# Optimization experiments

Hardware: AMD Instinct MI355X
Metric: run time of the kernel (lower is better)

## Reference

```python
import jax, jax.numpy as jnp
import numpy as np

N = 4096      # batch of RNA sequences
SEQ = 41      # hardcoded sequence length in the torch code
VEC = 15      # vector_length
T = 8         # target_length
EMB = 32      # embedding_dim of RNASequenceFilter.fc
LDIM = 256    # SequenceSplitter embedding_dim
RED = 64      # SequenceSplitter reduced_dim
BN_EPS = 1e-5


def setup_inputs() -> dict:
    key = jax.random.key(0)
    ks = jax.random.split(key, 20)
    A = jax.random.normal(ks[0], (N, SEQ, VEC), jnp.float32)
    start = jax.random.randint(ks[1], (N,), 0, 34)
    length = jax.random.randint(ks[2], (N,), 1, 9)  # region length in [1,8]
    C = jnp.stack([start, start + length - 1], axis=1).astype(jnp.int32)
    L = jax.random.normal(ks[3], (N, SEQ, LDIM), jnp.float32)
    s = 0.05
    return {
        "A": A, "C": C, "L": L,
        # RNASequenceFilter.fc : Linear(120,32) + Tanh + BatchNorm1d(32) (training mode)
        "W1": jax.random.normal(ks[4], (T * VEC, EMB), jnp.float32) * s,
        "b1": jnp.zeros((EMB,), jnp.float32),
        "bn_gamma": jnp.ones((EMB,), jnp.float32),
        "bn_beta": jnp.zeros((EMB,), jnp.float32),
        "sigma": jnp.float32(1.0),
        # SequenceSplitter lazy weights, initialized to ones
        "Pos_weights": jnp.ones((N, SEQ), jnp.float32),
        "Neg_weights": jnp.ones((N, SEQ), jnp.float32),
        # fc_pos
        "Wp1": jax.random.normal(ks[5], (LDIM, RED), jnp.float32) * s,
        "bp1": jnp.zeros((RED,), jnp.float32),
        "Wp2": jax.random.normal(ks[6], (RED, RED), jnp.float32) * s,
        "bp2": jnp.zeros((RED,), jnp.float32),
        # fc_neg
        "Wq1": jax.random.normal(ks[7], (LDIM, RED), jnp.float32) * s,
        "bq1": jnp.zeros((RED,), jnp.float32),
        "Wq2": jax.random.normal(ks[8], (RED, RED), jnp.float32) * s,
        "bq2": jnp.zeros((RED,), jnp.float32),
        # fc_all
        "Wa": jax.random.normal(ks[9], (LDIM, RED), jnp.float32) * s,
        "ba": jnp.zeros((RED,), jnp.float32),
    }


def _safe_cdist(x, y):
    # Euclidean cdist with zero (not NaN) gradient at zero distance.
    sq = (jnp.sum(x * x, -1)[:, None] + jnp.sum(y * y, -1)[None, :]
          - 2.0 * (x @ y.T))
    sq = jnp.maximum(sq, 0.0)
    safe = jnp.where(sq > 0.0, sq, 1.0)
    return jnp.where(sq > 0.0, jnp.sqrt(safe), 0.0)


def _forward(A, C, L, W1, b1, bn_gamma, bn_beta, sigma,
             Pos_weights, Neg_weights,
             Wp1, bp1, Wp2, bp2, Wq1, bq1, Wq2, bq2, Wa, ba):
    n = A.shape[0]
    start = C[:, 0].astype(jnp.int32)
    end = C[:, 1].astype(jnp.int32)
    length = end - start + 1  # [n], in [1, SEQ]

    # ---- build_graph: variable-length gather + linear interpolate (align_corners=False)
    j = jnp.arange(T, dtype=jnp.float32)
    scale = length.astype(jnp.float32)[:, None] / T          # [n,1]
    src = jnp.maximum(scale * (j + 0.5) - 0.5, 0.0)           # [n,T]
    i0 = jnp.minimum(jnp.floor(src).astype(jnp.int32), (length - 1)[:, None])
    i1 = jnp.minimum(i0 + 1, (length - 1)[:, None])
    w = src - i0.astype(jnp.float32)                          # lerp weight
    rows = jnp.arange(n)[:, None]
    g0 = A[rows, start[:, None] + i0]                         # [n,T,VEC]
    g1 = A[rows, start[:, None] + i1]
    key_regions = (1.0 - w)[..., None] * g0 + w[..., None] * g1
    flat = key_regions.reshape(n, T * VEC)

    h = jnp.tanh(flat @ W1 + b1)
    mu = h.mean(axis=0)
    var = ((h - mu) ** 2).mean(axis=0)                        # biased, training-mode BN
    emb = bn_gamma * (h - mu) * jax.lax.rsqrt(var + BN_EPS) + bn_beta

    D = jnp.exp(-_safe_cdist(emb, emb) / (2.0 * sigma ** 2))
    eye = jnp.eye(n, dtype=bool)
    off = ~eye
    avg = jnp.sum(jnp.where(off, D, 0.0)) / (n * (n - 1))
    D = jnp.where(D < avg, 0.0, D)
    mn = jnp.min(jnp.where(off, D, jnp.inf))
    mx = jnp.max(jnp.where(off, D, -jnp.inf))
    mx = jnp.where(mx == mn, mn + 1.0, mx)
    D = (D - mn) / (mx - mn)
    D = jnp.where(eye, 1.0, D)

    # ---- SequenceSplitter (only the paths feeding the outputs)
    idx = jnp.arange(SEQ)
    pmask = ((idx[None, :] >= start[:, None]) &
             (idx[None, :] <= end[:, None])).astype(L.dtype)  # [n,SEQ]
    pos_rep = (pmask * Pos_weights)[..., None] * L            # [n,SEQ,LDIM]
    neg_rep = ((1.0 - pmask) * Neg_weights)[..., None] * L

    key_t = jnp.tanh(jnp.tanh(pos_rep @ Wp1 + bp1) @ Wp2 + bp2)
    pos_vec = key_t.mean(axis=1)                              # [n,RED]
    nonkey_t = jnp.tanh(jnp.tanh(neg_rep @ Wq1 + bq1) @ Wq2 + bq2)
    neg_vec = nonkey_t.mean(axis=1)

    pos_sim = jnp.sum(jnp.exp(-_safe_cdist(pos_vec, pos_vec)))
    neg_sim = jnp.sum(jnp.exp(-_safe_cdist(pos_vec, neg_vec)))
    contrastive_loss = -jnp.log(pos_sim / neg_sim)

    final_feature = jnp.tanh((pos_rep + neg_rep) @ Wa + ba).mean(axis=1)  # [n,RED]
    return final_feature, contrastive_loss, D


def reference(A, C, L, W1, b1, bn_gamma, bn_beta, sigma,
              Pos_weights, Neg_weights,
              Wp1, bp1, Wp2, bp2, Wq1, bq1, Wq2, bq2, Wa, ba):
    return _forward(A, C, L, W1, b1, bn_gamma, bn_beta, sigma,
                    Pos_weights, Neg_weights,
                    Wp1, bp1, Wp2, bp2, Wq1, bq1, Wq2, bq2, Wa, ba)
```

## Files before the change

### kernel.cpp

```cpp
#include <hip/hip_runtime.h>
#include <cmath>

#define NN 4096
#define SEQ 41
#define VEC 15
#define TT 8
#define EMBD 32
#define LDIM 256
#define RED 64

#define WS_H       0
#define WS_EMB     524288
#define WS_SQN     1048576
#define WS_ROWSUM  1064960
#define WS_ROWMIN  1081344
#define WS_ROWMAX  1097728
#define WS_POSV    1114112
#define WS_NEGV    2162688
#define WS_STATS   3211264
#define WS_SIMS    3211520
#define WS_PAR     3211536

#define OUT_LOSS  (NN*RED)
#define OUT_D     (NN*RED + 1)

__global__ void k_init(char* ws) {
  double* sims = (double*)(ws + WS_SIMS);
  sims[0] = 0.0; sims[1] = 0.0;
}

__global__ __launch_bounds__(64) void k_interp_h(
    const float* __restrict__ A, const int* __restrict__ C,
    const float* __restrict__ W1, const float* __restrict__ b1,
    float* __restrict__ h)
{
  __shared__ float flat[TT*VEC];
  const int n = blockIdx.x;
  const int t = threadIdx.x;
  const int st = C[2*n], en = C[2*n+1];
  const int len = en - st + 1;
  const float scale = __fdiv_rn((float)len, 8.0f);
  const float* Arow = A + ((size_t)n*SEQ + st) * VEC;
  for (int idx = t; idx < TT*VEC; idx += 64) {
    int j = idx / VEC, k = idx - j*VEC;
    float jf = (float)j + 0.5f;
    float src = fmaxf(__fsub_rn(__fmul_rn(scale, jf), 0.5f), 0.0f);
    int i0 = min((int)floorf(src), len-1);
    int i1 = min(i0+1, len-1);
    float w = __fsub_rn(src, (float)i0);
    float g0 = Arow[i0*VEC + k];
    float g1 = Arow[i1*VEC + k];
    flat[idx] = __fadd_rn(__fmul_rn(__fsub_rn(1.0f, w), g0), __fmul_rn(w, g1));
  }
  __syncthreads();
  if (t < EMBD) {
    float acc = 0.0f;
    #pragma unroll
    for (int i = 0; i < TT*VEC; i++) acc = __fmaf_rn(flat[i], W1[i*EMBD + t], acc);
    acc = __fadd_rn(acc, b1[t]);
    h[(size_t)n*EMBD + t] = (float)tanh((double)acc);
  }
}

#define BCH 128
__global__ __launch_bounds__(256) void k_bnstats(const float* __restrict__ h,
                                                 float* __restrict__ stats)
{
  __shared__ float tile[2][BCH*EMBD];
  __shared__ float smu[32];
  const int t = threadIdx.x;
  const int NCH = NN / BCH;

  {
    const float4* src = (const float4*)h;
    float4* dst = (float4*)tile[0];
    for (int v = t; v < BCH*8; v += 256) dst[v] = src[v];
  }
  __syncthreads();
  float acc = 0.0f;
  for (int c = 0; c < NCH; c++) {
    if (t >= 64 && c+1 < NCH) {
      const float4* src = (const float4*)(h + (size_t)(c+1)*BCH*EMBD);
      float4* dst = (float4*)tile[(c+1)&1];
      for (int v = t-64; v < BCH*8; v += 192) dst[v] = src[v];
    }
    if (t < 32) {
      const float* p = tile[c&1];
      #pragma unroll 8
      for (int r = 0; r < BCH; r++) acc = __fadd_rn(acc, p[r*EMBD + t]);
    }
    __syncthreads();
  }
  if (t < 32) smu[t] = __fdiv_rn(acc, 4096.0f);
  __syncthreads();

  {
    const float4* src = (const float4*)h;
    float4* dst = (float4*)tile[0];
    for (int v = t; v < BCH*8; v += 256) dst[v] = src[v];
  }
  __syncthreads();
  float q = 0.0f;
  for (int c = 0; c < NCH; c++) {
    if (t >= 64 && c+1 < NCH) {
      const float4* src = (const float4*)(h + (size_t)(c+1)*BCH*EMBD);
      float4* dst = (float4*)tile[(c+1)&1];
      for (int v = t-64; v < BCH*8; v += 192) dst[v] = src[v];
    }
    if (t < 32) {
      const float* p = tile[c&1];
      const float m = smu[t];
      #pragma unroll 8
      for (int r = 0; r < BCH; r++) {
        float d = __fsub_rn(p[r*EMBD + t], m);
        q = __fadd_rn(q, __fmul_rn(d, d));
      }
    }
    __syncthreads();
  }
  if (t < 32) {
    float var = __fdiv_rn(q, 4096.0f);
    stats[t] = smu[t];
    stats[32+t] = __fdiv_rn(1.0f, __fsqrt_rn(__fadd_rn(var, 1e-5f)));
  }
}

__global__ __launch_bounds__(256) void k_emb(
    const float* __restrict__ h, const float* __restrict__ stats,
    const float* __restrict__ gamma, const float* __restrict__ beta,
    float* __restrict__ emb, float* __restrict__ sqn)
{
  __shared__ float tile[8][32];
  const int t = threadIdx.x;
  const int r = t >> 5;
  const int e = t & 31;
  const int n = blockIdx.x*8 + r;
  float hv = h[(size_t)n*EMBD + e];
  float v = __fadd_rn(__fmul_rn(__fmul_rn(gamma[e], __fsub_rn(hv, stats[e])), stats[32+e]), beta[e]);
  emb[(size_t)n*EMBD + e] = v;
  tile[r][e] = v;
  __syncthreads();
  if (e == 0) {
    float sq[32];
    #pragma unroll
    for (int k = 0; k < 32; k++) { float x = tile[r][k]; sq[k] = __fmul_rn(x, x); }
    float rr[8];
    #pragma unroll
    for (int m = 0; m < 8; m++) rr[m] = sq[m];
    #pragma unroll
    for (int g = 1; g < 4; g++)
      #pragma unroll
      for (int m = 0; m < 8; m++) rr[m] = __fadd_rn(rr[m], sq[8*g + m]);
    float a = __fadd_rn(__fadd_rn(rr[0], rr[1]), __fadd_rn(rr[2], rr[3]));
    float b = __fadd_rn(__fadd_rn(rr[4], rr[5]), __fadd_rn(rr[6], rr[7]));
    sqn[n] = __fadd_rn(a, b);
  }
}

__device__ __forceinline__ float finishD(float dot, float ni, float nj, float denom)
{
  float t1 = __fadd_rn(ni, nj);
  float sq = __fsub_rn(t1, __fmul_rn(2.0f, dot));
  sq = fmaxf(sq, 0.0f);
  float dist = (sq > 0.0f) ? __fsqrt_rn(sq) : 0.0f;
  float q = __fdiv_rn(-dist, denom);
  return (float)exp((double)q);
}

#define TI 64
#define TJ 128
__global__ __launch_bounds__(256) void k_dtile(
    const float* __restrict__ emb, const float* __restrict__ sqn,
    const float* __restrict__ sigma, float* __restrict__ Dout)
{
  __shared__ __align__(16) float Ei[TI][36];
  __shared__ __align__(16) float Ej[TJ][36];
  const int t = threadIdx.x;
  const int bi = blockIdx.y;
  const int bj = blockIdx.x;
  const int jt = t & 15;
  const int it = t >> 4;

  {
    const float4* si = (const float4*)(emb + (size_t)bi*TI*EMBD);
    for (int v = t; v < TI*8; v += 256) {
      float4 x = si[v];
      *(float4*)&Ei[v >> 3][(v & 7) * 4] = x;
    }
    const float4* sj = (const float4*)(emb + (size_t)bj*TJ*EMBD);
    for (int v = t; v < TJ*8; v += 256) {
      float4 x = sj[v];
      *(float4*)&Ej[v >> 3][(v & 7) * 4] = x;
    }
  }

  const float s0 = sigma[0];
  const float denom = __fmul_rn(2.0f, __fmul_rn(s0, s0));

  float ni[4], nj[8];
  #pragma unroll
  for (int r = 0; r < 4; r++) ni[r] = sqn[bi*TI + it*4 + r];
  #pragma unroll
  for (int u = 0; u < 8; u++) nj[u] = sqn[bj*TJ + jt + 16*u];

  __syncthreads();

  float acc[4][8];
  #pragma unroll
  for (int r = 0; r < 4; r++)
    #pragma unroll
    for (int u = 0; u < 8; u++) acc[r][u] = 0.0f;

  #pragma unroll
  for (int kq = 0; kq < 8; kq++) {
    float4 a[4], b[8];
    #pragma unroll
    for (int r = 0; r < 4; r++) a[r] = *(const float4*)&Ei[it*4 + r][kq*4];
    #pragma unroll
    for (int u = 0; u < 8; u++) b[u] = *(const float4*)&Ej[jt + 16*u][kq*4];
    #pragma unroll
    for (int r = 0; r < 4; r++)
      #pragma unroll
      for (int u = 0; u < 8; u++) {
        float s = acc[r][u];
        s = __fmaf_rn(a[r].x, b[u].x, s);
        s = __fmaf_rn(a[r].y, b[u].y, s);
        s = __fmaf_rn(a[r].z, b[u].z, s);
        s = __fmaf_rn(a[r].w, b[u].w, s);
        acc[r][u] = s;
      }
  }

  #pragma unroll
  for (int r = 0; r < 4; r++) {
    const int ig = bi*TI + it*4 + r;
    float* Dr = Dout + (size_t)ig * NN + bj*TJ;
    #pragma unroll
    for (int u = 0; u < 8; u++) {
      const int jg = bj*TJ + jt + 16*u;
      float Dv = finishD(acc[r][u], ni[r], nj[u], denom);
      Dr[jt + 16*u] = (jg == ig) ? 0.0f : Dv;
    }
  }
}

__global__ __launch_bounds__(256) void k_drowsum(
    const float* __restrict__ Dout,
    float* __restrict__ rowsum, float* __restrict__ rowmin, float* __restrict__ rowmax)
{
  __shared__ float Drow[NN + NN/128];
  __shared__ float cs[32];
  __shared__ float rmn[256], rmx[256];
  const int i = blockIdx.x;
  const int t = threadIdx.x;
  const float* Dr = Dout + (size_t)i*NN;
  const float PINF = __int_as_float(0x7f800000);
  const float NINF = __int_as_float(0xff800000);
  float lmn = PINF, lmx = NINF;
  for (int j = t; j < NN; j += 256) {
    float v = Dr[j];
    Drow[j + (j>>7)] = v;
    if (j != i) { lmn = fminf(lmn, v); lmx = fmaxf(lmx, v); }
  }
  rmn[t] = lmn; rmx[t] = lmx;
  __syncthreads();
  if (t < 32) {
    const float* p = Drow + 129*t;
    float rr[8];
    #pragma unroll
    for (int m = 0; m < 8; m++) rr[m] = p[m];
    for (int g = 1; g < 16; g++)
      #pragma unroll
      for (int m = 0; m < 8; m++) rr[m] = __fadd_rn(rr[m], p[8*g + m]);
    float a = __fadd_rn(__fadd_rn(rr[0], rr[1]), __fadd_rn(rr[2], rr[3]));
    float b = __fadd_rn(__fadd_rn(rr[4], rr[5]), __fadd_rn(rr[6], rr[7]));
    cs[t] = __fadd_rn(a, b);
  }
  __syncthreads();
  if (t == 0) {
    for (int len = 32; len > 1; len >>= 1)
      for (int k = 0; k < len/2; k++)
        cs[k] = __fadd_rn(cs[2*k], cs[2*k+1]);
    rowsum[i] = cs[0];
  }
  for (int s = 128; s > 0; s >>= 1) {
    if (t < s) {
      rmn[t] = fminf(rmn[t], rmn[t+s]);
      rmx[t] = fmaxf(rmx[t], rmx[t+s]);
    }
    __syncthreads();
  }
  if (t == 0) { rowmin[i] = rmn[0]; rowmax[i] = rmx[0]; }
}

__global__ __launch_bounds__(256) void k_dreduce(
    const float* __restrict__ rowsum, const float* __restrict__ rowmin,
    const float* __restrict__ rowmax, float* __restrict__ par)
{
  __shared__ float s[8192];
  __shared__ float rmn[256], rmx[256];
  const int t = threadIdx.x;
  for (int k = t; k < NN; k += 256) s[k] = rowsum[k];
  float mn = __int_as_float(0x7f800000), mx = __int_as_float(0xff800000);
  for (int k = t; k < NN; k += 256) {
    mn = fminf(mn, rowmin[k]);
    mx = fmaxf(mx, rowmax[k]);
  }
  rmn[t] = mn; rmx[t] = mx;
  __syncthreads();
  int src = 0, dst = 4096;
  for (int len = NN; len > 1; len >>= 1) {
    for (int k = t; k < len/2; k += 256)
      s[dst + k] = __fadd_rn(s[src + 2*k], s[src + 2*k+1]);
    __syncthreads();
    src = dst; dst = src + len/2;
  }
  for (int w = 128; w > 0; w >>= 1) {
    if (t < w) {
      rmn[t] = fminf(rmn[t], rmn[t+w]);
      rmx[t] = fmaxf(rmx[t], rmx[t+w]);
    }
    __syncthreads();
  }
  if (t == 0) {
    float S = s[src];
    float avg = __fdiv_rn(S, 16773120.0f);
    float mnr = rmn[0], mxr = rmx[0];
    float mnt = (mnr < avg) ? 0.0f : mnr;
    float mxt = (mxr < avg) ? 0.0f : mxr;
    if (mxt == mnt) mxt = __fadd_rn(mnt, 1.0f);
    par[0] = avg; par[1] = mnt; par[2] = __fsub_rn(mxt, mnt);
  }
}

__global__ __launch_bounds__(256) void k_dnorm(
    const float* __restrict__ par, float* __restrict__ D)
{
  const int i = blockIdx.x;
  const int t = threadIdx.x;
  const float avg = par[0], mnt = par[1], rng = par[2];
  float4* row = (float4*)(D + (size_t)i*NN);
  const int iv = i >> 2;
  for (int v = t; v < NN/4; v += 256) {
    float4 d = row[v];
    float o[4];
    float in[4] = {d.x, d.y, d.z, d.w};
    #pragma unroll
    for (int u = 0; u < 4; u++) {
      float val = (in[u] < avg) ? 0.0f : in[u];
      o[u] = __fdiv_rn(__fsub_rn(val, mnt), rng);
    }
    if (v == iv) o[i & 3] = 1.0f;
    row[v] = make_float4(o[0], o[1], o[2], o[3]);
  }
}

__global__ __launch_bounds__(256) void k_lpass(
    const float* __restrict__ L, const int* __restrict__ C,
    const float* __restrict__ PosW, const float* __restrict__ NegW,
    const float* __restrict__ Wp1, const float* __restrict__ bp1,
    const float* __restrict__ Wp2, const float* __restrict__ bp2,
    const float* __restrict__ Wq1, const float* __restrict__ bq1,
    const float* __restrict__ Wq2, const float* __restrict__ bq2,
    const float* __restrict__ Wa, const float* __restrict__ ba,
    float* __restrict__ out_ff, float* __restrict__ posv, float* __restrict__ negv)
{
  __shared__ __align__(16) float buf[SEQ*128];
  __shared__ float wps[SEQ], wns[SEQ];
  __shared__ float part[12*64];

  float* apos = buf;
  float* aneg = buf + SEQ*RED;

  const int n = blockIdx.x;
  const int t = threadIdx.x;
  const int w = t >> 6;
  const int lane = t & 63;

  if (t < SEQ) {
    int st = C[2*n], en = C[2*n+1];
    bool pm = (t >= st && t <= en);
    wps[t] = pm ? PosW[(size_t)n*SEQ + t] : 0.0f;
    wns[t] = pm ? 0.0f : NegW[(size_t)n*SEQ + t];
  }

  float accp[11], accq[11], acca[11];
  #pragma unroll
  for (int i = 0; i < 11; i++) { accp[i]=0.f; accq[i]=0.f; acca[i]=0.f; }

  const float4* Lg = (const float4*)(L + (size_t)n * (SEQ*LDIM));

  #pragma unroll
  for (int half = 0; half < 2; half++) {
    {
      float4* B4 = (float4*)buf;
      for (int v = t; v < SEQ*32; v += 256) {
        int s = v >> 5, c = v & 31;
        B4[v] = Lg[s*64 + half*32 + c];
      }
    }
    __syncthreads();
    const float* Wp1h = Wp1 + (size_t)half*128*RED + lane;
    const float* Wq1h = Wq1 + (size_t)half*128*RED + lane;
    const float* Wah  = Wa  + (size_t)half*128*RED + lane;
    for (int k0 = 0; k0 < 128; k0 += 4) {
      float wpr[4], wqr[4], war[4];
      #pragma unroll
      for (int kk = 0; kk < 4; kk++) {
        wpr[kk] = Wp1h[(k0+kk)*RED];
        wqr[kk] = Wq1h[(k0+kk)*RED];
        war[kk] = Wah [(k0+kk)*RED];
      }
      #pragma unroll
      for (int si = 0; si < 11; si++) {
        int s = w + 4*si;
        if (s < SEQ) {
          float4 l4 = *(const float4*)&buf[s*128 + k0];
          accp[si] = __fmaf_rn(l4.x, wpr[0], accp[si]);
          accp[si] = __fmaf_rn(l4.y, wpr[1], accp[si]);
          accp[si] = __fmaf_rn(l4.z, wpr[2], accp[si]);
          accp[si] = __fmaf_rn(l4.w, wpr[3], accp[si]);
          accq[si] = __fmaf_rn(l4.x, wqr[0], accq[si]);
          accq[si] = __fmaf_rn(l4.y, wqr[1], accq[si]);
          accq[si] = __fmaf_rn(l4.z, wqr[2], accq[si]);
          accq[si] = __fmaf_rn(l4.w, wqr[3], accq[si]);
          acca[si] = __fmaf_rn(l4.x, war[0], acca[si]);
          acca[si] = __fmaf_rn(l4.y, war[1], acca[si]);
          acca[si] = __fmaf_rn(l4.z, war[2], acca[si]);
          acca[si] = __fmaf_rn(l4.w, war[3], acca[si]);
        }
      }
    }
    __syncthreads();
  }

  const float bpl = bp1[lane], bql = bq1[lane], bal = ba[lane];
  float ffl = 0.f;
  #pragma unroll
  for (int si = 0; si < 11; si++) {
    int s = w + 4*si;
    if (s < SEQ) {
      float wp = wps[s], wn = wns[s];
      apos[s*RED + lane] = tanhf(__fmaf_rn(wp, accp[si], bpl));
      aneg[s*RED + lane] = tanhf(__fmaf_rn(wn, accq[si], bql));
      ffl += tanhf(__fmaf_rn(wp+wn, acca[si], bal));
    }
  }
  part[(0*4 + w)*64 + lane] = ffl;
  __syncthreads();

  float accP[11], accQ[11];
  #pragma unroll
  for (int i = 0; i < 11; i++) { accP[i]=0.f; accQ[i]=0.f; }
  const float* Wp2l = Wp2 + lane;
  const float* Wq2l = Wq2 + lane;
  for (int k0 = 0; k0 < RED; k0 += 4) {
    float p2[4], q2[4];
    #pragma unroll
    for (int kk = 0; kk < 4; kk++) {
      p2[kk] = Wp2l[(k0+kk)*RED];
      q2[kk] = Wq2l[(k0+kk)*RED];
    }
    #pragma unroll
    for (int si = 0; si < 11; si++) {
      int s = w + 4*si;
      if (s < SEQ) {
        float4 a4 = *(const float4*)&apos[s*RED + k0];
        float4 b4 = *(const float4*)&aneg[s*RED + k0];
        accP[si] = __fmaf_rn(a4.x, p2[0], accP[si]);
        accP[si] = __fmaf_rn(a4.y, p2[1], accP[si]);
        accP[si] = __fmaf_rn(a4.z, p2[2], accP[si]);
        accP[si] = __fmaf_rn(a4.w, p2[3], accP[si]);
        accQ[si] = __fmaf_rn(b4.x, q2[0], accQ[si]);
        accQ[si] = __fmaf_rn(b4.y, q2[1], accQ[si]);
        accQ[si] = __fmaf_rn(b4.z, q2[2], accQ[si]);
        accQ[si] = __fmaf_rn(b4.w, q2[3], accQ[si]);
      }
    }
  }
  const float bp2l = bp2[lane], bq2l = bq2[lane];
  float pl = 0.f, nl = 0.f;
  #pragma unroll
  for (int si = 0; si < 11; si++) {
    int s = w + 4*si;
    if (s < SEQ) {
      pl += tanhf(__fadd_rn(accP[si], bp2l));
      nl += tanhf(__fadd_rn(accQ[si], bq2l));
    }
  }
  part[(1*4 + w)*64 + lane] = pl;
  part[(2*4 + w)*64 + lane] = nl;
  __syncthreads();

  if (w == 0) {
    float s = part[0*256 + 0*64 + lane] + part[0*256 + 1*64 + lane]
            + part[0*256 + 2*64 + lane] + part[0*256 + 3*64 + lane];
    out_ff[(size_t)n*RED + lane] = s * (1.0f/41.0f);
  } else if (w == 1) {
    float s = part[1*256 + 0*64 + lane] + part[1*256 + 1*64 + lane]
            + part[1*256 + 2*64 + lane] + part[1*256 + 3*64 + lane];
    posv[(size_t)n*RED + lane] = s * (1.0f/41.0f);
  } else if (w == 2) {
    float s = part[2*256 + 0*64 + lane] + part[2*256 + 1*64 + lane]
            + part[2*256 + 2*64 + lane] + part[2*256 + 3*64 + lane];
    negv[(size_t)n*RED + lane] = s * (1.0f/41.0f);
  }
}

__global__ __launch_bounds__(256) void k_sim(
    const float* __restrict__ posv, const float* __restrict__ negv,
    double* __restrict__ sims)
{
  __shared__ float xI[64*64];
  __shared__ float yJ[64*65];
  __shared__ float nxs[64];
  __shared__ double wsum[4];
  const int which = blockIdx.z;
  const float* X = posv;
  const float* Y = which ? negv : posv;
  const int bi = blockIdx.x, bj = blockIdx.y, t = threadIdx.x;
  for (int v = t; v < 4096; v += 256) {
    int r = v >> 6, c = v & 63;
    xI[r*64+c] = X[(size_t)(bi*64+r)*RED + c];
    yJ[r*65+c] = Y[(size_t)(bj*64+r)*RED + c];
  }
  __syncthreads();
  if (t < 64) {
    float s = 0.f;
    #pragma unroll
    for (int k = 0; k < 64; k++) { float v = xI[t*64+k]; s += v*v; }
    nxs[t] = s;
  }
  const int jl = t & 63, iq = t >> 6;
  float yv[64];
  #pragma unroll
  for (int k = 0; k < 64; k++) yv[k] = yJ[jl*65+k];
  float ny = 0.f;
  #pragma unroll
  for (int k = 0; k < 64; k++) ny += yv[k]*yv[k];
  __syncthreads();
  double lsum = 0.0;
  for (int ii = 0; ii < 16; ii++) {
    int il = iq*16 + ii;
    float dot = 0.f;
    #pragma unroll
    for (int k = 0; k < 64; k += 4) {
      float4 x = *(const float4*)&xI[il*64+k];
      dot += x.x*yv[k] + x.y*yv[k+1] + x.z*yv[k+2] + x.w*yv[k+3];
    }
    float sq = fmaxf(nxs[il] + ny - 2.0f*dot, 0.0f);
    float dist = (sq > 0.f) ? sqrtf(sq) : 0.f;
    lsum += (double)expf(-dist);
  }
  #pragma unroll
  for (int m = 32; m >= 1; m >>= 1) lsum += __shfl_down(lsum, m);
  if ((t & 63) == 0) wsum[t>>6] = lsum;
  __syncthreads();
  if (t == 0) atomicAdd(&sims[which], wsum[0]+wsum[1]+wsum[2]+wsum[3]);
}

__global__ void k_loss(const double* __restrict__ sims, float* __restrict__ out_loss) {
  out_loss[0] = (float)(-log(sims[0]/sims[1]));
}

extern "C" void kernel_launch(void* const* d_in, const int* in_sizes, int n_in,
                              void* d_out, int out_size, void* d_ws, size_t ws_size,
                              hipStream_t stream) {
  const float* A     = (const float*)d_in[0];
  const int*   C     = (const int*)  d_in[1];
  const float* L     = (const float*)d_in[2];
  const float* W1    = (const float*)d_in[3];
  const float* b1    = (const float*)d_in[4];
  const float* gamma = (const float*)d_in[5];
  const float* beta  = (const float*)d_in[6];
  const float* sigma = (const float*)d_in[7];
  const float* PosW  = (const float*)d_in[8];
  const float* NegW  = (const float*)d_in[9];
  const float* Wp1   = (const float*)d_in[10];
  const float* bp1   = (const float*)d_in[11];
  const float* Wp2   = (const float*)d_in[12];
  const float* bp2   = (const float*)d_in[13];
  const float* Wq1   = (const float*)d_in[14];
  const float* bq1   = (const float*)d_in[15];
  const float* Wq2   = (const float*)d_in[16];
  const float* bq2   = (const float*)d_in[17];
  const float* Wa    = (const float*)d_in[18];
  const float* ba    = (const float*)d_in[19];

  float* out = (float*)d_out;
  char* ws = (char*)d_ws;
  float* h      = (float*)(ws + WS_H);
  float* emb    = (float*)(ws + WS_EMB);
  float* sqn    = (float*)(ws + WS_SQN);
  float* rowsum = (float*)(ws + WS_ROWSUM);
  float* rowmin = (float*)(ws + WS_ROWMIN);
  float* rowmax = (float*)(ws + WS_ROWMAX);
  float* posv   = (float*)(ws + WS_POSV);
  float* negv   = (float*)(ws + WS_NEGV);
  float* stats  = (float*)(ws + WS_STATS);
  double* sims  = (double*)(ws + WS_SIMS);
  float* par    = (float*)(ws + WS_PAR);

  hipLaunchKernelGGL(k_init, dim3(1), dim3(1), 0, stream, (char*)d_ws);
  hipLaunchKernelGGL(k_interp_h, dim3(NN), dim3(64), 0, stream, A, C, W1, b1, h);
  hipLaunchKernelGGL(k_bnstats, dim3(1), dim3(256), 0, stream, h, stats);
  hipLaunchKernelGGL(k_emb, dim3(NN/8), dim3(256), 0, stream, h, stats, gamma, beta, emb, sqn);
  hipLaunchKernelGGL(k_dtile, dim3(NN/TJ, NN/TI), dim3(256), 0, stream, emb, sqn, sigma, out + OUT_D);
  hipLaunchKernelGGL(k_drowsum, dim3(NN), dim3(256), 0, stream, out + OUT_D, rowsum, rowmin, rowmax);
  hipLaunchKernelGGL(k_dreduce, dim3(1), dim3(256), 0, stream, rowsum, rowmin, rowmax, par);
  hipLaunchKernelGGL(k_dnorm, dim3(NN), dim3(256), 0, stream, par, out + OUT_D);
  hipLaunchKernelGGL(k_lpass, dim3(NN), dim3(256), 0, stream,
                     L, C, PosW, NegW, Wp1, bp1, Wp2, bp2, Wq1, bq1, Wq2, bq2, Wa, ba,
                     out, posv, negv);
  hipLaunchKernelGGL(k_sim, dim3(64,64,2), dim3(256), 0, stream, posv, negv, sims);
  hipLaunchKernelGGL(k_loss, dim3(1), dim3(1), 0, stream, sims, out + OUT_LOSS);
}
```

Before: 892.3 us.

## Fuse D row reductions into tile kernel, skip masked branch work, halve symmetric sim

Per-row sum, min and max of the distance matrix are now computed inside the tile kernel via wave shuffles and atomics, with per-chunk partial sums combined by a small kernel. This removes the separate pass that re-read the full 4096x4096 D matrix. The L-pass now runs only the positive or the negative branch per sequence position, and replaces the masked-out branch with a precomputed constant tanh term. The positive-positive similarity kernel skips the lower-triangle blocks and doubles the off-diagonal ones, which changes the float summation order, and the init kernel is folded into the combine kernel.

Measured after the change: 942.3 us. 1.06x slower.

```diff
diff --git a/kernel.cpp b/kernel.cpp
--- a/kernel.cpp
+++ b/kernel.cpp
@@ -10,6 +10,7 @@
 #define RED 64
 
 #define WS_H       0
+#define WS_CHUNKS  0
 #define WS_EMB     524288
 #define WS_SQN     1048576
 #define WS_ROWSUM  1064960
@@ -23,11 +24,6 @@
 
 #define OUT_LOSS  (NN*RED)
 #define OUT_D     (NN*RED + 1)
-
-__global__ void k_init(char* ws) {
-  double* sims = (double*)(ws + WS_SIMS);
-  sims[0] = 0.0; sims[1] = 0.0;
-}
 
 __global__ __launch_bounds__(64) void k_interp_h(
     const float* __restrict__ A, const int* __restrict__ C,
@@ -128,7 +124,8 @@
 __global__ __launch_bounds__(256) void k_emb(
     const float* __restrict__ h, const float* __restrict__ stats,
     const float* __restrict__ gamma, const float* __restrict__ beta,
-    float* __restrict__ emb, float* __restrict__ sqn)
+    float* __restrict__ emb, float* __restrict__ sqn,
+    float* __restrict__ rowmin, float* __restrict__ rowmax)
 {
   __shared__ float tile[8][32];
   const int t = threadIdx.x;
@@ -154,6 +151,8 @@
     float a = __fadd_rn(__fadd_rn(rr[0], rr[1]), __fadd_rn(rr[2], rr[3]));
     float b = __fadd_rn(__fadd_rn(rr[4], rr[5]), __fadd_rn(rr[6], rr[7]));
     sqn[n] = __fadd_rn(a, b);
+    rowmin[n] = __int_as_float(0x7f800000);
+    rowmax[n] = 0.0f;
   }
 }
 
@@ -171,7 +170,8 @@
 #define TJ 128
 __global__ __launch_bounds__(256) void k_dtile(
     const float* __restrict__ emb, const float* __restrict__ sqn,
-    const float* __restrict__ sigma, float* __restrict__ Dout)
+    const float* __restrict__ sigma, float* __restrict__ Dout,
+    float* __restrict__ chunks, float* __restrict__ rowmin, float* __restrict__ rowmax)
 {
   __shared__ __align__(16) float Ei[TI][36];
   __shared__ __align__(16) float Ej[TJ][36];
@@ -231,66 +231,74 @@
       }
   }
 
+  const float PINF = __int_as_float(0x7f800000);
+  const float NINF = __int_as_float(0xff800000);
+  float wv[4][8];
+  float thmn[4], thmx[4];
   #pragma unroll
   for (int r = 0; r < 4; r++) {
     const int ig = bi*TI + it*4 + r;
     float* Dr = Dout + (size_t)ig * NN + bj*TJ;
+    float mn = PINF, mx = NINF;
     #pragma unroll
     for (int u = 0; u < 8; u++) {
       const int jg = bj*TJ + jt + 16*u;
       float Dv = finishD(acc[r][u], ni[r], nj[u], denom);
-      Dr[jt + 16*u] = (jg == ig) ? 0.0f : Dv;
-    }
-  }
-}
-
-__global__ __launch_bounds__(256) void k_drowsum(
-    const float* __restrict__ Dout,
-    float* __restrict__ rowsum, float* __restrict__ rowmin, float* __restrict__ rowmax)
-{
-  __shared__ float Drow[NN + NN/128];
-  __shared__ float cs[32];
-  __shared__ float rmn[256], rmx[256];
-  const int i = blockIdx.x;
-  const int t = threadIdx.x;
-  const float* Dr = Dout + (size_t)i*NN;
-  const float PINF = __int_as_float(0x7f800000);
-  const float NINF = __int_as_float(0xff800000);
-  float lmn = PINF, lmx = NINF;
-  for (int j = t; j < NN; j += 256) {
-    float v = Dr[j];
-    Drow[j + (j>>7)] = v;
-    if (j != i) { lmn = fminf(lmn, v); lmx = fmaxf(lmx, v); }
-  }
-  rmn[t] = lmn; rmx[t] = lmx;
-  __syncthreads();
-  if (t < 32) {
-    const float* p = Drow + 129*t;
-    float rr[8];
-    #pragma unroll
-    for (int m = 0; m < 8; m++) rr[m] = p[m];
-    for (int g = 1; g < 16; g++)
-      #pragma unroll
-      for (int m = 0; m < 8; m++) rr[m] = __fadd_rn(rr[m], p[8*g + m]);
-    float a = __fadd_rn(__fadd_rn(rr[0], rr[1]), __fadd_rn(rr[2], rr[3]));
-    float b = __fadd_rn(__fadd_rn(rr[4], rr[5]), __fadd_rn(rr[6], rr[7]));
-    cs[t] = __fadd_rn(a, b);
-  }
-  __syncthreads();
-  if (t == 0) {
-    for (int len = 32; len > 1; len >>= 1)
-      for (int k = 0; k < len/2; k++)
-        cs[k] = __fadd_rn(cs[2*k], cs[2*k+1]);
-    rowsum[i] = cs[0];
-  }
-  for (int s = 128; s > 0; s >>= 1) {
-    if (t < s) {
-      rmn[t] = fminf(rmn[t], rmn[t+s]);
-      rmx[t] = fmaxf(rmx[t], rmx[t+s]);
-    }
-    __syncthreads();
-  }
-  if (t == 0) { rowmin[i] = rmn[0]; rowmax[i] = rmx[0]; }
+      const bool dg = (jg == ig);
+      float wq = dg ? 0.0f : Dv;
+      wv[r][u] = wq;
+      Dr[jt + 16*u] = wq;
+      mn = fminf(mn, dg ? PINF : Dv);
+      mx = fmaxf(mx, dg ? NINF : Dv);
+    }
+    thmn[r] = mn; thmx[r] = mx;
+  }
+
+  #pragma unroll
+  for (int r = 0; r < 4; r++) {
+    float part[8];
+    #pragma unroll
+    for (int u = 0; u < 8; u++) part[u] = __shfl_xor(wv[r][u], 8, 16);
+    float a = wv[r][0];
+    a = __fadd_rn(a, part[0]);
+    #pragma unroll
+    for (int u = 1; u < 8; u++) {
+      a = __fadd_rn(a, wv[r][u]);
+      a = __fadd_rn(a, part[u]);
+    }
+    float s1 = __fadd_rn(a,  __shfl_xor(a, 1, 16));
+    float s2 = __fadd_rn(s1, __shfl_xor(s1, 2, 16));
+    float s3 = __fadd_rn(s2, __shfl_xor(s2, 4, 16));
+    float mn = thmn[r], mx = thmx[r];
+    #pragma unroll
+    for (int m = 1; m < 16; m <<= 1) {
+      mn = fminf(mn, __shfl_xor(mn, m, 16));
+      mx = fmaxf(mx, __shfl_xor(mx, m, 16));
+    }
+    if (jt == 0) {
+      const int ig = bi*TI + it*4 + r;
+      chunks[(size_t)bj*NN + ig] = s3;
+      atomicMin((int*)&rowmin[ig], __float_as_int(mn));
+      atomicMax((int*)&rowmax[ig], __float_as_int(mx));
+    }
+  }
+}
+
+__global__ __launch_bounds__(256) void k_rowcombine(
+    const float* __restrict__ chunks, float* __restrict__ rowsum,
+    double* __restrict__ sims)
+{
+  const int i = blockIdx.x*256 + threadIdx.x;
+  if (blockIdx.x == 0 && threadIdx.x == 0) { sims[0] = 0.0; sims[1] = 0.0; }
+  float ch[32];
+  #pragma unroll
+  for (int c = 0; c < 32; c++) ch[c] = chunks[(size_t)c*NN + i];
+  #pragma unroll
+  for (int len = 32; len > 1; len >>= 1)
+    #pragma unroll
+    for (int k = 0; k < 16; k++)
+      if (k < len/2) ch[k] = __fadd_rn(ch[2*k], ch[2*k+1]);
+  rowsum[i] = ch[0];
 }
 
 __global__ __launch_bounds__(256) void k_dreduce(
@@ -368,25 +376,36 @@
   __shared__ __align__(16) float buf[SEQ*128];
   __shared__ float wps[SEQ], wns[SEQ];
   __shared__ float part[12*64];
+  __shared__ __align__(16) float tb1[2*RED];
 
   float* apos = buf;
   float* aneg = buf + SEQ*RED;
 
   const int n = blockIdx.x;
   const int t = threadIdx.x;
-  const int w = t >> 6;
+  const int wu = __builtin_amdgcn_readfirstlane(t >> 6);
   const int lane = t & 63;
 
+  const int st = C[2*n], en = C[2*n+1];
+
   if (t < SEQ) {
-    int st = C[2*n], en = C[2*n+1];
     bool pm = (t >= st && t <= en);
     wps[t] = pm ? PosW[(size_t)n*SEQ + t] : 0.0f;
     wns[t] = pm ? 0.0f : NegW[(size_t)n*SEQ + t];
   }
-
-  float accp[11], accq[11], acca[11];
-  #pragma unroll
-  for (int i = 0; i < 11; i++) { accp[i]=0.f; accq[i]=0.f; acca[i]=0.f; }
+  if (t < RED) tb1[t] = tanhf(bp1[t]);
+  else if (t < 2*RED) tb1[t] = tanhf(bq1[t - RED]);
+
+  bool anyIn = false, anyOut = false;
+  #pragma unroll
+  for (int si = 0; si < 11; si++) {
+    int s = wu + 4*si;
+    if (s < SEQ) { bool r = (s >= st) && (s <= en); anyIn |= r; anyOut |= !r; }
+  }
+
+  float accs[11], acca[11];
+  #pragma unroll
+  for (int i = 0; i < 11; i++) { accs[i]=0.f; acca[i]=0.f; }
 
   const float4* Lg = (const float4*)(L + (size_t)n * (SEQ*LDIM));
 
@@ -405,25 +424,33 @@
     const float* Wah  = Wa  + (size_t)half*128*RED + lane;
     for (int k0 = 0; k0 < 128; k0 += 4) {
       float wpr[4], wqr[4], war[4];
+      if (anyIn) {
+        #pragma unroll
+        for (int kk = 0; kk < 4; kk++) wpr[kk] = Wp1h[(k0+kk)*RED];
+      }
+      if (anyOut) {
+        #pragma unroll
+        for (int kk = 0; kk < 4; kk++) wqr[kk] = Wq1h[(k0+kk)*RED];
+      }
       #pragma unroll
-      for (int kk = 0; kk < 4; kk++) {
-        wpr[kk] = Wp1h[(k0+kk)*RED];
-        wqr[kk] = Wq1h[(k0+kk)*RED];
-        war[kk] = Wah [(k0+kk)*RED];
-      }
+      for (int kk = 0; kk < 4; kk++) war[kk] = Wah[(k0+kk)*RED];
       #pragma unroll
       for (int si = 0; si < 11; si++) {
-        int s = w + 4*si;
+        const int s = wu + 4*si;
         if (s < SEQ) {
+          const bool inr = (s >= st) && (s <= en);
           float4 l4 = *(const float4*)&buf[s*128 + k0];
-          accp[si] = __fmaf_rn(l4.x, wpr[0], accp[si]);
-          accp[si] = __fmaf_rn(l4.y, wpr[1], accp[si]);
-          accp[si] = __fmaf_rn(l4.z, wpr[2], accp[si]);
-          accp[si] = __fmaf_rn(l4.w, wpr[3], accp[si]);
-          accq[si] = __fmaf_rn(l4.x, wqr[0], accq[si]);
-          accq[si] = __fmaf_rn(l4.y, wqr[1], accq[si]);
-          accq[si] = __fmaf_rn(l4.z, wqr[2], accq[si]);
-          accq[si] = __fmaf_rn(l4.w, wqr[3], accq[si]);
+          if (inr) {
+            accs[si] = __fmaf_rn(l4.x, wpr[0], accs[si]);
+            accs[si] = __fmaf_rn(l4.y, wpr[1], accs[si]);
+            accs[si] = __fmaf_rn(l4.z, wpr[2], accs[si]);
+            accs[si] = __fmaf_rn(l4.w, wpr[3], accs[si]);
+          } else {
+            accs[si] = __fmaf_rn(l4.x, wqr[0], accs[si]);
+            accs[si] = __fmaf_rn(l4.y, wqr[1], accs[si]);
+            accs[si] = __fmaf_rn(l4.z, wqr[2], accs[si]);
+            accs[si] = __fmaf_rn(l4.w, wqr[3], accs[si]);
+          }
           acca[si] = __fmaf_rn(l4.x, war[0], acca[si]);
           acca[si] = __fmaf_rn(l4.y, war[1], acca[si]);
           acca[si] = __fmaf_rn(l4.z, war[2], acca[si]);
@@ -438,20 +465,27 @@
   float ffl = 0.f;
   #pragma unroll
   for (int si = 0; si < 11; si++) {
-    int s = w + 4*si;
+    const int s = wu + 4*si;
     if (s < SEQ) {
-      float wp = wps[s], wn = wns[s];
-      apos[s*RED + lane] = tanhf(__fmaf_rn(wp, accp[si], bpl));
-      aneg[s*RED + lane] = tanhf(__fmaf_rn(wn, accq[si], bql));
-      ffl += tanhf(__fmaf_rn(wp+wn, acca[si], bal));
-    }
-  }
-  part[(0*4 + w)*64 + lane] = ffl;
-  __syncthreads();
-
-  float accP[11], accQ[11];
-  #pragma unroll
-  for (int i = 0; i < 11; i++) { accP[i]=0.f; accQ[i]=0.f; }
+      const bool inr = (s >= st) && (s <= en);
+      if (inr) {
+        float wp = wps[s];
+        apos[s*RED + lane] = tanhf(__fmaf_rn(wp, accs[si], bpl));
+        ffl += tanhf(__fmaf_rn(wp, acca[si], bal));
+      } else {
+        float wn = wns[s];
+        aneg[s*RED + lane] = tanhf(__fmaf_rn(wn, accs[si], bql));
+        ffl += tanhf(__fmaf_rn(wn, acca[si], bal));
+      }
+    }
+  }
+  part[(0*4 + wu)*64 + lane] = ffl;
+  __syncthreads();
+
+  float acc2[11];
+  float c2p = 0.f, c2q = 0.f;
+  #pragma unroll
+  for (int i = 0; i < 11; i++) acc2[i] = 0.f;
   const float* Wp2l = Wp2 + lane;
   const float* Wq2l = Wq2 + lane;
   for (int k0 = 0; k0 < RED; k0 += 4) {
@@ -461,46 +495,71 @@
       p2[kk] = Wp2l[(k0+kk)*RED];
       q2[kk] = Wq2l[(k0+kk)*RED];
     }
+    float4 tp = *(const float4*)&tb1[k0];
+    float4 tq = *(const float4*)&tb1[RED + k0];
+    c2p = __fmaf_rn(tp.x, p2[0], c2p);
+    c2p = __fmaf_rn(tp.y, p2[1], c2p);
+    c2p = __fmaf_rn(tp.z, p2[2], c2p);
+    c2p = __fmaf_rn(tp.w, p2[3], c2p);
+    c2q = __fmaf_rn(tq.x, q2[0], c2q);
+    c2q = __fmaf_rn(tq.y, q2[1], c2q);
+    c2q = __fmaf_rn(tq.z, q2[2], c2q);
+    c2q = __fmaf_rn(tq.w, q2[3], c2q);
     #pragma unroll
     for (int si = 0; si < 11; si++) {
-      int s = w + 4*si;
+      const int s = wu + 4*si;
       if (s < SEQ) {
-        float4 a4 = *(const float4*)&apos[s*RED + k0];
-        float4 b4 = *(const float4*)&aneg[s*RED + k0];
-        accP[si] = __fmaf_rn(a4.x, p2[0], accP[si]);
-        accP[si] = __fmaf_rn(a4.y, p2[1], accP[si]);
-        accP[si] = __fmaf_rn(a4.z, p2[2], accP[si]);
-        accP[si] = __fmaf_rn(a4.w, p2[3], accP[si]);
-        accQ[si] = __fmaf_rn(b4.x, q2[0], accQ[si]);
-        accQ[si] = __fmaf_rn(b4.y, q2[1], accQ[si]);
-        accQ[si] = __fmaf_rn(b4.z, q2[2], accQ[si]);
-        accQ[si] = __fmaf_rn(b4.w, q2[3], accQ[si]);
+        const bool inr = (s >= st) && (s <= en);
+        if (inr) {
+          float4 a4 = *(const float4*)&apos[s*RED + k0];
+          acc2[si] = __fmaf_rn(a4.x, p2[0], acc2[si]);
+          acc2[si] = __fmaf_rn(a4.y, p2[1], acc2[si]);
+          acc2[si] = __fmaf_rn(a4.z, p2[2], acc2[si]);
+          acc2[si] = __fmaf_rn(a4.w, p2[3], acc2[si]);
+        } else {
+          float4 b4 = *(const float4*)&aneg[s*RED + k0];
+          acc2[si] = __fmaf_rn(b4.x, q2[0], acc2[si]);
+          acc2[si] = __fmaf_rn(b4.y, q2[1], acc2[si]);
+          acc2[si] = __fmaf_rn(b4.z, q2[2], acc2[si]);
+          acc2[si] = __fmaf_rn(b4.w, q2[3], acc2[si]);
+        }
       }
     }
   }
   const float bp2l = bp2[lane], bq2l = bq2[lane];
+  const float tcp = tanhf(__fadd_rn(c2p, bp2l));
+  const float tcq = tanhf(__fadd_rn(c2q, bq2l));
   float pl = 0.f, nl = 0.f;
+  int nin = 0, nval = 0;
   #pragma unroll
   for (int si = 0; si < 11; si++) {
-    int s = w + 4*si;
+    const int s = wu + 4*si;
     if (s < SEQ) {
-      pl += tanhf(__fadd_rn(accP[si], bp2l));
-      nl += tanhf(__fadd_rn(accQ[si], bq2l));
-    }
-  }
-  part[(1*4 + w)*64 + lane] = pl;
-  part[(2*4 + w)*64 + lane] = nl;
-  __syncthreads();
-
-  if (w == 0) {
+      nval++;
+      const bool inr = (s >= st) && (s <= en);
+      if (inr) {
+        nin++;
+        pl += tanhf(__fadd_rn(acc2[si], bp2l));
+      } else {
+        nl += tanhf(__fadd_rn(acc2[si], bq2l));
+      }
+    }
+  }
+  pl += (float)(nval - nin) * tcp;
+  nl += (float)nin * tcq;
+  part[(1*4 + wu)*64 + lane] = pl;
+  part[(2*4 + wu)*64 + lane] = nl;
+  __syncthreads();
+
+  if (wu == 0) {
     float s = part[0*256 + 0*64 + lane] + part[0*256 + 1*64 + lane]
             + part[0*256 + 2*64 + lane] + part[0*256 + 3*64 + lane];
     out_ff[(size_t)n*RED + lane] = s * (1.0f/41.0f);
-  } else if (w == 1) {
+  } else if (wu == 1) {
     float s = part[1*256 + 0*64 + lane] + part[1*256 + 1*64 + lane]
             + part[1*256 + 2*64 + lane] + part[1*256 + 3*64 + lane];
     posv[(size_t)n*RED + lane] = s * (1.0f/41.0f);
-  } else if (w == 2) {
+  } else if (wu == 2) {
     float s = part[2*256 + 0*64 + lane] + part[2*256 + 1*64 + lane]
             + part[2*256 + 2*64 + lane] + part[2*256 + 3*64 + lane];
     negv[(size_t)n*RED + lane] = s * (1.0f/41.0f);
@@ -516,12 +575,17 @@
   __shared__ float nxs[64];
   __shared__ double wsum[4];
   const int which = blockIdx.z;
+  const int bi = blockIdx.x, bj = blockIdx.y, t = threadIdx.x;
+  if (which == 0 && bi > bj) return;
   const float* X = posv;
   const float* Y = which ? negv : posv;
-  const int bi = blockIdx.x, bj = blockIdx.y, t = threadIdx.x;
+  {
+    const float4* X4 = (const float4*)(X + (size_t)(bi*64)*RED);
+    float4* xI4 = (float4*)xI;
+    for (int v = t; v < 1024; v += 256) xI4[v] = X4[v];
+  }
   for (int v = t; v < 4096; v += 256) {
     int r = v >> 6, c = v & 63;
-    xI[r*64+c] = X[(size_t)(bi*64+r)*RED + c];
     yJ[r*65+c] = Y[(size_t)(bj*64+r)*RED + c];
   }
   __syncthreads();
@@ -556,7 +620,10 @@
   for (int m = 32; m >= 1; m >>= 1) lsum += __shfl_down(lsum, m);
   if ((t & 63) == 0) wsum[t>>6] = lsum;
   __syncthreads();
-  if (t == 0) atomicAdd(&sims[which], wsum[0]+wsum[1]+wsum[2]+wsum[3]);
+  if (t == 0) {
+    double mult = (which == 0 && bi < bj) ? 2.0 : 1.0;
+    atomicAdd(&sims[which], mult*(wsum[0]+wsum[1]+wsum[2]+wsum[3]));
+  }
 }
 
 __global__ void k_loss(const double* __restrict__ sims, float* __restrict__ out_loss) {
@@ -590,6 +657,7 @@
   float* out = (float*)d_out;
   char* ws = (char*)d_ws;
   float* h      = (float*)(ws + WS_H);
+  float* chunks = (float*)(ws + WS_CHUNKS);
   float* emb    = (float*)(ws + WS_EMB);
   float* sqn    = (float*)(ws + WS_SQN);
   float* rowsum = (float*)(ws + WS_ROWSUM);
@@ -601,12 +669,11 @@
   double* sims  = (double*)(ws + WS_SIMS);
   float* par    = (float*)(ws + WS_PAR);
 
-  hipLaunchKernelGGL(k_init, dim3(1), dim3(1), 0, stream, (char*)d_ws);
   hipLaunchKernelGGL(k_interp_h, dim3(NN), dim3(64), 0, stream, A, C, W1, b1, h);
   hipLaunchKernelGGL(k_bnstats, dim3(1), dim3(256), 0, stream, h, stats);
-  hipLaunchKernelGGL(k_emb, dim3(NN/8), dim3(256), 0, stream, h, stats, gamma, beta, emb, sqn);
-  hipLaunchKernelGGL(k_dtile, dim3(NN/TJ, NN/TI), dim3(256), 0, stream, emb, sqn, sigma, out + OUT_D);
-  hipLaunchKernelGGL(k_drowsum, dim3(NN), dim3(256), 0, stream, out + OUT_D, rowsum, rowmin, rowmax);
+  hipLaunchKernelGGL(k_emb, dim3(NN/8), dim3(256), 0, stream, h, stats, gamma, beta, emb, sqn, rowmin, rowmax);
+  hipLaunchKernelGGL(k_dtile, dim3(NN/TJ, NN/TI), dim3(256), 0, stream, emb, sqn, sigma, out + OUT_D, chunks, rowmin, rowmax);
+  hipLaunchKernelGGL(k_rowcombine, dim3(16), dim3(256), 0, stream, chunks, rowsum, sims);
   hipLaunchKernelGGL(k_dreduce, dim3(1), dim3(256), 0, stream, rowsum, rowmin, rowmax, par);
   hipLaunchKernelGGL(k_dnorm, dim3(NN), dim3(256), 0, stream, par, out + OUT_D);
   hipLaunchKernelGGL(k_lpass, dim3(NN), dim3(256), 0, stream,
```

## Recompute distance tiles instead of storing and rereading the full D matrix

Applied to the files above, without the earlier changes.

The first distance-tile pass no longer writes the 4096x4096 D matrix. It reduces per-row partial sums and min/max in registers and shuffles, storing chunk sums plus atomic min/max. A second tile pass recomputes the distances and writes the normalized output once, replacing the separate row-sum and normalize passes that each read the full matrix. The similarity kernel also skips the lower triangle for the symmetric pos/pos case, and the init kernel is folded into the row-combine kernel. This trades roughly two extra 64MB passes over D for duplicated cheap compute, but relies on rowmax being initialized to 0 with int-bit atomics on non-negative floats, and the chunk-sum summation order differs from before.

Result: slower. 979.7 us (+9.8%).

```diff
diff --git a/kernel.cpp b/kernel.cpp
--- a/kernel.cpp
+++ b/kernel.cpp
@@ -10,6 +10,7 @@
 #define RED 64
 
 #define WS_H       0
+#define WS_CHUNKS  0
 #define WS_EMB     524288
 #define WS_SQN     1048576
 #define WS_ROWSUM  1064960
@@ -23,11 +24,6 @@
 
 #define OUT_LOSS  (NN*RED)
 #define OUT_D     (NN*RED + 1)
-
-__global__ void k_init(char* ws) {
-  double* sims = (double*)(ws + WS_SIMS);
-  sims[0] = 0.0; sims[1] = 0.0;
-}
 
 __global__ __launch_bounds__(64) void k_interp_h(
     const float* __restrict__ A, const int* __restrict__ C,
@@ -128,7 +124,8 @@
 __global__ __launch_bounds__(256) void k_emb(
     const float* __restrict__ h, const float* __restrict__ stats,
     const float* __restrict__ gamma, const float* __restrict__ beta,
-    float* __restrict__ emb, float* __restrict__ sqn)
+    float* __restrict__ emb, float* __restrict__ sqn,
+    float* __restrict__ rowmin, float* __restrict__ rowmax)
 {
   __shared__ float tile[8][32];
   const int t = threadIdx.x;
@@ -154,6 +151,8 @@
     float a = __fadd_rn(__fadd_rn(rr[0], rr[1]), __fadd_rn(rr[2], rr[3]));
     float b = __fadd_rn(__fadd_rn(rr[4], rr[5]), __fadd_rn(rr[6], rr[7]));
     sqn[n] = __fadd_rn(a, b);
+    rowmin[n] = __int_as_float(0x7f800000);
+    rowmax[n] = 0.0f;
   }
 }
 
@@ -171,7 +170,8 @@
 #define TJ 128
 __global__ __launch_bounds__(256) void k_dtile(
     const float* __restrict__ emb, const float* __restrict__ sqn,
-    const float* __restrict__ sigma, float* __restrict__ Dout)
+    const float* __restrict__ sigma,
+    float* __restrict__ chunks, float* __restrict__ rowmin, float* __restrict__ rowmax)
 {
   __shared__ __align__(16) float Ei[TI][36];
   __shared__ __align__(16) float Ej[TJ][36];
@@ -231,66 +231,71 @@
       }
   }
 
+  const float PINF = __int_as_float(0x7f800000);
+  const float NINF = __int_as_float(0xff800000);
+  float wv[4][8];
+  float thmn[4], thmx[4];
   #pragma unroll
   for (int r = 0; r < 4; r++) {
     const int ig = bi*TI + it*4 + r;
-    float* Dr = Dout + (size_t)ig * NN + bj*TJ;
+    float mn = PINF, mx = NINF;
     #pragma unroll
     for (int u = 0; u < 8; u++) {
       const int jg = bj*TJ + jt + 16*u;
       float Dv = finishD(acc[r][u], ni[r], nj[u], denom);
-      Dr[jt + 16*u] = (jg == ig) ? 0.0f : Dv;
-    }
-  }
-}
-
-__global__ __launch_bounds__(256) void k_drowsum(
-    const float* __restrict__ Dout,
-    float* __restrict__ rowsum, float* __restrict__ rowmin, float* __restrict__ rowmax)
-{
-  __shared__ float Drow[NN + NN/128];
-  __shared__ float cs[32];
-  __shared__ float rmn[256], rmx[256];
-  const int i = blockIdx.x;
-  const int t = threadIdx.x;
-  const float* Dr = Dout + (size_t)i*NN;
-  const float PINF = __int_as_float(0x7f800000);
-  const float NINF = __int_as_float(0xff800000);
-  float lmn = PINF, lmx = NINF;
-  for (int j = t; j < NN; j += 256) {
-    float v = Dr[j];
-    Drow[j + (j>>7)] = v;
-    if (j != i) { lmn = fminf(lmn, v); lmx = fmaxf(lmx, v); }
-  }
-  rmn[t] = lmn; rmx[t] = lmx;
-  __syncthreads();
-  if (t < 32) {
-    const float* p = Drow + 129*t;
-    float rr[8];
-    #pragma unroll
-    for (int m = 0; m < 8; m++) rr[m] = p[m];
-    for (int g = 1; g < 16; g++)
-      #pragma unroll
-      for (int m = 0; m < 8; m++) rr[m] = __fadd_rn(rr[m], p[8*g + m]);
-    float a = __fadd_rn(__fadd_rn(rr[0], rr[1]), __fadd_rn(rr[2], rr[3]));
-    float b = __fadd_rn(__fadd_rn(rr[4], rr[5]), __fadd_rn(rr[6], rr[7]));
-    cs[t] = __fadd_rn(a, b);
-  }
-  __syncthreads();
-  if (t == 0) {
-    for (int len = 32; len > 1; len >>= 1)
-      for (int k = 0; k < len/2; k++)
-        cs[k] = __fadd_rn(cs[2*k], cs[2*k+1]);
-    rowsum[i] = cs[0];
-  }
-  for (int s = 128; s > 0; s >>= 1) {
-    if (t < s) {
-      rmn[t] = fminf(rmn[t], rmn[t+s]);
-      rmx[t] = fmaxf(rmx[t], rmx[t+s]);
-    }
-    __syncthreads();
-  }
-  if (t == 0) { rowmin[i] = rmn[0]; rowmax[i] = rmx[0]; }
+      const bool dg = (jg == ig);
+      wv[r][u] = dg ? 0.0f : Dv;
+      mn = fminf(mn, dg ? PINF : Dv);
+      mx = fmaxf(mx, dg ? NINF : Dv);
+    }
+    thmn[r] = mn; thmx[r] = mx;
+  }
+
+  #pragma unroll
+  for (int r = 0; r < 4; r++) {
+    float part[8];
+    #pragma unroll
+    for (int u = 0; u < 8; u++) part[u] = __shfl_xor(wv[r][u], 8, 16);
+    float a = wv[r][0];
+    a = __fadd_rn(a, part[0]);
+    #pragma unroll
+    for (int u = 1; u < 8; u++) {
+      a = __fadd_rn(a, wv[r][u]);
+      a = __fadd_rn(a, part[u]);
+    }
+    float s1 = __fadd_rn(a,  __shfl_xor(a, 1, 16));
+    float s2 = __fadd_rn(s1, __shfl_xor(s1, 2, 16));
+    float s3 = __fadd_rn(s2, __shfl_xor(s2, 4, 16));
+    float mn = thmn[r], mx = thmx[r];
+    #pragma unroll
+    for (int m = 1; m < 16; m <<= 1) {
+      mn = fminf(mn, __shfl_xor(mn, m, 16));
+      mx = fmaxf(mx, __shfl_xor(mx, m, 16));
+    }
+    if (jt == 0) {
+      const int ig = bi*TI + it*4 + r;
+      chunks[(size_t)bj*NN + ig] = s3;
+      atomicMin((int*)&rowmin[ig], __float_as_int(mn));
+      atomicMax((int*)&rowmax[ig], __float_as_int(mx));
+    }
+  }
+}
+
+__global__ __launch_bounds__(256) void k_rowcombine(
+    const float* __restrict__ chunks, float* __restrict__ rowsum,
+    double* __restrict__ sims)
+{
+  const int i = blockIdx.x*256 + threadIdx.x;
+  if (blockIdx.x == 0 && threadIdx.x == 0) { sims[0] = 0.0; sims[1] = 0.0; }
+  float ch[32];
+  #pragma unroll
+  for (int c = 0; c < 32; c++) ch[c] = chunks[(size_t)c*NN + i];
+  #pragma unroll
+  for (int len = 32; len > 1; len >>= 1)
+    #pragma unroll
+    for (int k = 0; k < 16; k++)
+      if (k < len/2) ch[k] = __fadd_rn(ch[2*k], ch[2*k+1]);
+  rowsum[i] = ch[0];
 }
 
 __global__ __launch_bounds__(256) void k_dreduce(
@@ -333,25 +338,82 @@
   }
 }
 
-__global__ __launch_bounds__(256) void k_dnorm(
-    const float* __restrict__ par, float* __restrict__ D)
-{
-  const int i = blockIdx.x;
+__global__ __launch_bounds__(256) void k_dstore(
+    const float* __restrict__ emb, const float* __restrict__ sqn,
+    const float* __restrict__ sigma, const float* __restrict__ par,
+    float* __restrict__ Dout)
+{
+  __shared__ __align__(16) float Ei[TI][36];
+  __shared__ __align__(16) float Ej[TJ][36];
   const int t = threadIdx.x;
+  const int bi = blockIdx.y;
+  const int bj = blockIdx.x;
+  const int jt = t & 15;
+  const int it = t >> 4;
+
+  {
+    const float4* si = (const float4*)(emb + (size_t)bi*TI*EMBD);
+    for (int v = t; v < TI*8; v += 256) {
+      float4 x = si[v];
+      *(float4*)&Ei[v >> 3][(v & 7) * 4] = x;
+    }
+    const float4* sj = (const float4*)(emb + (size_t)bj*TJ*EMBD);
+    for (int v = t; v < TJ*8; v += 256) {
+      float4 x = sj[v];
+      *(float4*)&Ej[v >> 3][(v & 7) * 4] = x;
+    }
+  }
+
+  const float s0 = sigma[0];
+  const float denom = __fmul_rn(2.0f, __fmul_rn(s0, s0));
   const float avg = par[0], mnt = par[1], rng = par[2];
-  float4* row = (float4*)(D + (size_t)i*NN);
-  const int iv = i >> 2;
-  for (int v = t; v < NN/4; v += 256) {
-    float4 d = row[v];
-    float o[4];
-    float in[4] = {d.x, d.y, d.z, d.w};
-    #pragma unroll
-    for (int u = 0; u < 4; u++) {
-      float val = (in[u] < avg) ? 0.0f : in[u];
-      o[u] = __fdiv_rn(__fsub_rn(val, mnt), rng);
-    }
-    if (v == iv) o[i & 3] = 1.0f;
-    row[v] = make_float4(o[0], o[1], o[2], o[3]);
+
+  float ni[4], nj[8];
+  #pragma unroll
+  for (int r = 0; r < 4; r++) ni[r] = sqn[bi*TI + it*4 + r];
+  #pragma unroll
+  for (int u = 0; u < 8; u++) nj[u] = sqn[bj*TJ + jt + 16*u];
+
+  __syncthreads();
+
+  float acc[4][8];
+  #pragma unroll
+  for (int r = 0; r < 4; r++)
+    #pragma unroll
+    for (int u = 0; u < 8; u++) acc[r][u] = 0.0f;
+
+  #pragma unroll
+  for (int kq = 0; kq < 8; kq++) {
+    float4 a[4], b[8];
+    #pragma unroll
+    for (int r = 0; r < 4; r++) a[r] = *(const float4*)&Ei[it*4 + r][kq*4];
+    #pragma unroll
+    for (int u = 0; u < 8; u++) b[u] = *(const float4*)&Ej[jt + 16*u][kq*4];
+    #pragma unroll
+    for (int r = 0; r < 4; r++)
+      #pragma unroll
+      for (int u = 0; u < 8; u++) {
+        float s = acc[r][u];
+        s = __fmaf_rn(a[r].x, b[u].x, s);
+        s = __fmaf_rn(a[r].y, b[u].y, s);
+        s = __fmaf_rn(a[r].z, b[u].z, s);
+        s = __fmaf_rn(a[r].w, b[u].w, s);
+        acc[r][u] = s;
+      }
+  }
+
+  #pragma unroll
+  for (int r = 0; r < 4; r++) {
+    const int ig = bi*TI + it*4 + r;
+    float* Dr = Dout + (size_t)ig * NN + bj*TJ;
+    #pragma unroll
+    for (int u = 0; u < 8; u++) {
+      const int jg = bj*TJ + jt + 16*u;
+      float Dv = finishD(acc[r][u], ni[r], nj[u], denom);
+      float val = (Dv < avg) ? 0.0f : Dv;
+      float o = __fdiv_rn(__fsub_rn(val, mnt), rng);
+      Dr[jt + 16*u] = (jg == ig) ? 1.0f : o;
+    }
   }
 }
 
@@ -516,12 +578,17 @@
   __shared__ float nxs[64];
   __shared__ double wsum[4];
   const int which = blockIdx.z;
+  const int bi = blockIdx.x, bj = blockIdx.y, t = threadIdx.x;
+  if (which == 0 && bi > bj) return;
   const float* X = posv;
   const float* Y = which ? negv : posv;
-  const int bi = blockIdx.x, bj = blockIdx.y, t = threadIdx.x;
+  {
+    const float4* X4 = (const float4*)(X + (size_t)(bi*64)*RED);
+    float4* xI4 = (float4*)xI;
+    for (int v = t; v < 1024; v += 256) xI4[v] = X4[v];
+  }
   for (int v = t; v < 4096; v += 256) {
     int r = v >> 6, c = v & 63;
-    xI[r*64+c] = X[(size_t)(bi*64+r)*RED + c];
     yJ[r*65+c] = Y[(size_t)(bj*64+r)*RED + c];
   }
   __syncthreads();
@@ -556,7 +623,10 @@
   for (int m = 32; m >= 1; m >>= 1) lsum += __shfl_down(lsum, m);
   if ((t & 63) == 0) wsum[t>>6] = lsum;
   __syncthreads();
-  if (t == 0) atomicAdd(&sims[which], wsum[0]+wsum[1]+wsum[2]+wsum[3]);
+  if (t == 0) {
+    double mult = (which == 0 && bi < bj) ? 2.0 : 1.0;
+    atomicAdd(&sims[which], mult*(wsum[0]+wsum[1]+wsum[2]+wsum[3]));
+  }
 }
 
 __global__ void k_loss(const double* __restrict__ sims, float* __restrict__ out_loss) {
@@ -590,6 +660,7 @@
   float* out = (float*)d_out;
   char* ws = (char*)d_ws;
   float* h      = (float*)(ws + WS_H);
+  float* chunks = (float*)(ws + WS_CHUNKS);
   float* emb    = (float*)(ws + WS_EMB);
   float* sqn    = (float*)(ws + WS_SQN);
   float* rowsum = (float*)(ws + WS_ROWSUM);
@@ -601,14 +672,13 @@
   double* sims  = (double*)(ws + WS_SIMS);
   float* par    = (float*)(ws + WS_PAR);
 
-  hipLaunchKernelGGL(k_init, dim3(1), dim3(1), 0, stream, (char*)d_ws);
   hipLaunchKernelGGL(k_interp_h, dim3(NN), dim3(64), 0, stream, A, C, W1, b1, h);
   hipLaunchKernelGGL(k_bnstats, dim3(1), dim3(256), 0, stream, h, stats);
-  hipLaunchKernelGGL(k_emb, dim3(NN/8), dim3(256), 0, stream, h, stats, gamma, beta, emb, sqn);
-  hipLaunchKernelGGL(k_dtile, dim3(NN/TJ, NN/TI), dim3(256), 0, stream, emb, sqn, sigma, out + OUT_D);
-  hipLaunchKernelGGL(k_drowsum, dim3(NN), dim3(256), 0, stream, out + OUT_D, rowsum, rowmin, rowmax);
+  hipLaunchKernelGGL(k_emb, dim3(NN/8), dim3(256), 0, stream, h, stats, gamma, beta, emb, sqn, rowmin, rowmax);
+  hipLaunchKernelGGL(k_dtile, dim3(NN/TJ, NN/TI), dim3(256), 0, stream, emb, sqn, sigma, chunks, rowmin, rowmax);
+  hipLaunchKernelGGL(k_rowcombine, dim3(16), dim3(256), 0, stream, chunks, rowsum, sims);
   hipLaunchKernelGGL(k_dreduce, dim3(1), dim3(256), 0, stream, rowsum, rowmin, rowmax, par);
-  hipLaunchKernelGGL(k_dnorm, dim3(NN), dim3(256), 0, stream, par, out + OUT_D);
+  hipLaunchKernelGGL(k_dstore, dim3(NN/TJ, NN/TI), dim3(256), 0, stream, emb, sqn, sigma, par, out + OUT_D);
   hipLaunchKernelGGL(k_lpass, dim3(NN), dim3(256), 0, stream,
                      L, C, PosW, NegW, Wp1, bp1, Wp2, bp2, Wq1, bq1, Wq2, bq2, Wa, ba,
                      out, posv, negv);
```
